# Kernel tuning notes

Measured on AMD Instinct MI355X. Metric: run time of the kernel, lower is better.

The kernel has to match this reference:

```python
import jax, jax.numpy as jnp
import numpy as np

EMBED = 128
STATE = 64
HID = 160
VOCAB = 32000


def layer_norm(x, g, b, eps=1e-5):
    mu = x.mean(-1, keepdims=True)
    var = ((x - mu) ** 2).mean(-1, keepdims=True)
    return (x - mu) * jax.lax.rsqrt(var + eps) * g + b


def mamba_block(x, norm_g, norm_b, in_w, in_b, conv_w, conv_b,
                dt_w, dt_b, b_w, b_b, c_w, c_b, a_log, d, out_w, out_b):
    # x: [B,T,D]
    res = x
    xn = layer_norm(x, norm_g, norm_b)
    proj = xn @ in_w.T + in_b                      # [B,T,2D]
    x_proj, z = jnp.split(proj, 2, axis=-1)
    D = x_proj.shape[-1]
    # depthwise conv1d, kernel 3, same padding
    xc = jax.lax.conv_general_dilated(
        x_proj.transpose(0, 2, 1), conv_w[:, None, :],
        window_strides=(1,), padding=((1, 1),),
        feature_group_count=D,
        dimension_numbers=('NCH', 'OIH', 'NCH')) + conv_b[:, None]
    x_conv = jnp.tanh(xc.transpose(0, 2, 1))       # [B,T,D]
    # input-dependent SSM params, computed for all timesteps at once
    dt = jax.nn.softplus(z @ dt_w.T + dt_b) + 1e-4  # [B,T,S]
    bt = jnp.tanh(z @ b_w.T + b_b)                  # [B,T,S]
    ct = jnp.tanh(z @ c_w.T + c_b)                  # [B,T,S]
    a = -jnp.exp(a_log)                             # [S]
    decay = jnp.exp(a * dt)                         # [B,T,S]

    def step(state, inp):
        dec_t, b_t = inp
        state = state * dec_t + b_t
        return state, state

    state0 = jnp.zeros((x.shape[0], a_log.shape[0]), x.dtype)
    _, states = jax.lax.scan(step, state0,
                             (decay.transpose(1, 0, 2), bt.transpose(1, 0, 2)))
    y = ct * states.transpose(1, 0, 2)              # [B,T,S]
    mix = jnp.concatenate([x_conv * d, y], axis=-1)  # [B,T,D+S]
    return res + mix @ out_w.T + out_b


def _forward(x, lengths, resp_in, emb_table,
             m_norm_g, m_norm_b, m_in_w, m_in_b, m_conv_w, m_conv_b,
             m_dt_w, m_dt_b, m_b_w, m_b_b, m_c_w, m_c_b, m_a_log, m_d,
             m_out_w, m_out_b, pool_g, pool_b, shared_w, shared_b,
             intent_w, intent_b, style_w, style_b, cap_w, cap_b, op_w, op_b,
             dec_emb, dec_init_w, dec_init_b,
             gru_w_ih, gru_w_hh, gru_b_ih, gru_b_hh, dec_out_w, dec_out_b):
    emb = emb_table[x]                              # [B,T,E]
    h_seq = emb
    for i in range(2):
        h_seq = mamba_block(h_seq, m_norm_g[i], m_norm_b[i], m_in_w[i],
                            m_in_b[i], m_conv_w[i], m_conv_b[i], m_dt_w[i],
                            m_dt_b[i], m_b_w[i], m_b_b[i], m_c_w[i], m_c_b[i],
                            m_a_log[i], m_d[i], m_out_w[i], m_out_b[i])
    T = h_seq.shape[1]
    mask = (jnp.arange(T)[None, :] < lengths[:, None])[..., None]
    denom = jnp.maximum(lengths, 1)[:, None].astype(h_seq.dtype)
    pooled = (h_seq * mask).sum(axis=1) / denom     # [B,E]
    h = layer_norm(pooled, pool_g, pool_b)
    h = jax.nn.relu(h @ shared_w.T + shared_b)      # [B,128]
    intent = h @ intent_w.T + intent_b
    style = h @ style_w.T + style_b
    cap = h @ cap_w.T + cap_b
    op = h @ op_w.T + op_b
    # GRU decoder (PyTorch gate order: r, z, n)
    dec_in = dec_emb[resp_in]                       # [B,Td,E]
    h0 = jnp.tanh(h @ dec_init_w.T + dec_init_b)    # [B,H]
    gx = dec_in @ gru_w_ih.T + gru_b_ih             # [B,Td,3H]

    def gru_step(hprev, gx_t):
        gh = hprev @ gru_w_hh.T + gru_b_hh
        xr, xz, xn = jnp.split(gx_t, 3, axis=-1)
        hr, hz, hn = jnp.split(gh, 3, axis=-1)
        r = jax.nn.sigmoid(xr + hr)
        zg = jax.nn.sigmoid(xz + hz)
        n = jnp.tanh(xn + r * hn)
        hnew = (1.0 - zg) * n + zg * hprev
        return hnew, hnew

    _, dec_states = jax.lax.scan(gru_step, h0, gx.transpose(1, 0, 2))
    dec_out = dec_states.transpose(1, 0, 2)         # [B,Td,H]
    resp_logits = dec_out @ dec_out_w.T + dec_out_b  # [B,Td,V]
    return (intent, style, cap, op, resp_logits, h)


def setup_inputs() -> dict:
    key = jax.random.key(0)
    ks = iter(jax.random.split(key, 64))

    def nrm(shape, s=0.02):
        return jax.random.normal(next(ks), shape, jnp.float32) * s

    inp = {}
    inp['x'] = jax.random.randint(next(ks), (32, 512), 0, VOCAB)
    inp['lengths'] = jax.random.randint(next(ks), (32,), 1, 513)
    inp['resp_in'] = jax.random.randint(next(ks), (32, 128), 0, VOCAB)
    inp['emb_table'] = nrm((VOCAB, EMBED), 1.0).at[0].set(0.0)
    inp['m_norm_g'] = jnp.ones((2, EMBED)); inp['m_norm_b'] = jnp.zeros((2, EMBED))
    inp['m_in_w'] = nrm((2, 2 * EMBED, EMBED)); inp['m_in_b'] = jnp.zeros((2, 2 * EMBED))
    inp['m_conv_w'] = nrm((2, EMBED, 3), 0.1); inp['m_conv_b'] = jnp.zeros((2, EMBED))
    inp['m_dt_w'] = nrm((2, STATE, EMBED)); inp['m_dt_b'] = jnp.zeros((2, STATE))
    inp['m_b_w'] = nrm((2, STATE, EMBED)); inp['m_b_b'] = jnp.zeros((2, STATE))
    inp['m_c_w'] = nrm((2, STATE, EMBED)); inp['m_c_b'] = jnp.zeros((2, STATE))
    inp['m_a_log'] = nrm((2, STATE)); inp['m_d'] = jnp.ones((2, EMBED))
    inp['m_out_w'] = nrm((2, EMBED, EMBED + STATE)); inp['m_out_b'] = jnp.zeros((2, EMBED))
    inp['pool_g'] = jnp.ones((EMBED,)); inp['pool_b'] = jnp.zeros((EMBED,))
    inp['shared_w'] = nrm((128, EMBED)); inp['shared_b'] = jnp.zeros((128,))
    inp['intent_w'] = nrm((32, 128)); inp['intent_b'] = jnp.zeros((32,))
    inp['style_w'] = nrm((8, 128)); inp['style_b'] = jnp.zeros((8,))
    inp['cap_w'] = nrm((16, 128)); inp['cap_b'] = jnp.zeros((16,))
    inp['op_w'] = nrm((24, 128)); inp['op_b'] = jnp.zeros((24,))
    inp['dec_emb'] = nrm((VOCAB, EMBED), 1.0).at[0].set(0.0)
    inp['dec_init_w'] = nrm((HID, 128)); inp['dec_init_b'] = jnp.zeros((HID,))
    inp['gru_w_ih'] = nrm((3 * HID, EMBED)); inp['gru_w_hh'] = nrm((3 * HID, HID))
    inp['gru_b_ih'] = jnp.zeros((3 * HID,)); inp['gru_b_hh'] = jnp.zeros((3 * HID,))
    inp['dec_out_w'] = nrm((VOCAB, HID)); inp['dec_out_b'] = jnp.zeros((VOCAB,))
    return inp


def reference(x, lengths, resp_in, emb_table,
              m_norm_g, m_norm_b, m_in_w, m_in_b, m_conv_w, m_conv_b,
              m_dt_w, m_dt_b, m_b_w, m_b_b, m_c_w, m_c_b, m_a_log, m_d,
              m_out_w, m_out_b, pool_g, pool_b, shared_w, shared_b,
              intent_w, intent_b, style_w, style_b, cap_w, cap_b, op_w, op_b,
              dec_emb, dec_init_w, dec_init_b,
              gru_w_ih, gru_w_hh, gru_b_ih, gru_b_hh, dec_out_w, dec_out_b):
    return _forward(x, lengths, resp_in, emb_table,
                    m_norm_g, m_norm_b, m_in_w, m_in_b, m_conv_w, m_conv_b,
                    m_dt_w, m_dt_b, m_b_w, m_b_b, m_c_w, m_c_b, m_a_log, m_d,
                    m_out_w, m_out_b, pool_g, pool_b, shared_w, shared_b,
                    intent_w, intent_b, style_w, style_b, cap_w, cap_b,
                    op_w, op_b, dec_emb, dec_init_w, dec_init_b,
                    gru_w_ih, gru_w_hh, gru_b_ih, gru_b_hh,
                    dec_out_w, dec_out_b)
```

## Files before the change

### kernel.cpp

```cpp
#include <hip/hip_runtime.h>
#include <hip/hip_bf16.h>

#define EMBED 128
#define STATE 64
#define HID   160
#define VOCAB 32000
#define BDIM  32
#define TDIM  512
#define TDEC  128

typedef __attribute__((ext_vector_type(4))) float f32x4;
typedef __attribute__((ext_vector_type(8))) short bf16x8;

__device__ inline float softplus_f(float x) { return x > 20.f ? x : log1pf(expf(x)); }
__device__ inline float sigmoid_f(float x) { return 1.f / (1.f + expf(-x)); }
__device__ inline short f2bf(float x) {
    __hip_bfloat16 v = __float2bfloat16(x);
    return *reinterpret_cast<short*>(&v);
}
__device__ inline float bf2f(short u) {
    union { unsigned int i; float f; } cv;
    cv.i = ((unsigned int)(unsigned short)u) << 16;
    return cv.f;
}

__global__ void prep_kernel(const float* __restrict__ w, short* __restrict__ wb, int n,
                            const int* __restrict__ x, const int* __restrict__ lengths,
                            const int* __restrict__ resp, int* __restrict__ flags) {
    if (blockIdx.x == 0 && threadIdx.x == 0) {
        int f = 1;
        for (int i = 0; i < 32; i++) if (x[2 * i + 1] != 0) { f = 0; break; }
        flags[0] = f;
        f = 1;
        for (int i = 0; i < 16; i++) if (lengths[2 * i + 1] != 0) { f = 0; break; }
        flags[1] = f;
        f = 1;
        for (int i = 0; i < 32; i++) if (resp[2 * i + 1] != 0) { f = 0; break; }
        flags[2] = f;
    }
    int i = blockIdx.x * blockDim.x + threadIdx.x;
    int stride = gridDim.x * blockDim.x;
    for (; i < n; i += stride) wb[i] = f2bf(w[i]);
}

__global__ void embed_kernel(const int* __restrict__ tok, const float* __restrict__ table,
                             float* __restrict__ out, int total,
                             const int* __restrict__ flags, int fidx) {
    int mode = flags[fidx];
    int i = blockIdx.x * blockDim.x + threadIdx.x;
    int stride = gridDim.x * blockDim.x;
    for (; i < total; i += stride) {
        int r = i >> 7, e = i & 127;
        int t = mode ? tok[2 * r] : tok[r];
        out[i] = table[(long)t * EMBED + e];
    }
}

__launch_bounds__(256)
__global__ void mm_inproj(const float* __restrict__ hseq,
                          const float* __restrict__ g, const float* __restrict__ bta,
                          const float* __restrict__ W, const float* __restrict__ bias,
                          short* __restrict__ projb) {
    __shared__ __align__(16) short As[64][136];
    __shared__ __align__(16) short Ws[64][136];
    __shared__ float rsum[64][4], rsum2[64][4];
    const int m0 = blockIdx.x * 64, n0 = blockIdx.y * 64;
    const int tid = threadIdx.x;

    {
        int row = tid >> 2, part = tid & 3;
        const float* src = &hseq[(long)(m0 + row) * 128 + part * 32];
        f32x4 v[8];
        float s = 0.f, s2 = 0.f;
        #pragma unroll
        for (int q = 0; q < 8; q++) {
            v[q] = *(const f32x4*)&src[q * 4];
            s  += v[q].x + v[q].y + v[q].z + v[q].w;
            s2 += v[q].x * v[q].x + v[q].y * v[q].y + v[q].z * v[q].z + v[q].w * v[q].w;
        }
        rsum[row][part] = s; rsum2[row][part] = s2;
        __syncthreads();
        float tot  = rsum[row][0] + rsum[row][1] + rsum[row][2] + rsum[row][3];
        float tot2 = rsum2[row][0] + rsum2[row][1] + rsum2[row][2] + rsum2[row][3];
        float mu = tot * (1.f / 128.f);
        float var = tot2 * (1.f / 128.f) - mu * mu;
        float rstd = rsqrtf(var + 1e-5f);
        #pragma unroll
        for (int q = 0; q < 8; q++) {
            int c = part * 32 + q * 4;
            short4 t4;
            t4.x = f2bf((v[q].x - mu) * rstd * g[c + 0] + bta[c + 0]);
            t4.y = f2bf((v[q].y - mu) * rstd * g[c + 1] + bta[c + 1]);
            t4.z = f2bf((v[q].z - mu) * rstd * g[c + 2] + bta[c + 2]);
            t4.w = f2bf((v[q].w - mu) * rstd * g[c + 3] + bta[c + 3]);
            *(short4*)&As[row][c] = t4;
        }
    }
    #pragma unroll
    for (int it = 0; it < 4; ++it) {
        int idx = tid + it * 256;
        int rr = idx >> 4, cc = idx & 15;
        const float* wp = &W[(long)(n0 + rr) * 128 + cc * 8];
        short t8[8];
        #pragma unroll
        for (int q = 0; q < 8; q++) t8[q] = f2bf(wp[q]);
        *(bf16x8*)&Ws[rr][cc * 8] = *(bf16x8*)t8;
    }
    __syncthreads();

    const int wave = tid >> 6, lane = tid & 63;
    const int wm = wave >> 1, wn = wave & 1;
    const int fr = lane & 15, kg = lane >> 4;
    f32x4 acc[2][2];
    #pragma unroll
    for (int i = 0; i < 2; i++)
        #pragma unroll
        for (int j = 0; j < 2; j++) acc[i][j] = (f32x4){0.f, 0.f, 0.f, 0.f};
    #pragma unroll
    for (int ks = 0; ks < 4; ++ks) {
        int kb = ks * 32 + kg * 8;
        bf16x8 a0 = *(const bf16x8*)&As[wm * 32 + fr][kb];
        bf16x8 a1 = *(const bf16x8*)&As[wm * 32 + 16 + fr][kb];
        bf16x8 w0 = *(const bf16x8*)&Ws[wn * 32 + fr][kb];
        bf16x8 w1 = *(const bf16x8*)&Ws[wn * 32 + 16 + fr][kb];
        acc[0][0] = __builtin_amdgcn_mfma_f32_16x16x32_bf16(a0, w0, acc[0][0], 0, 0, 0);
        acc[0][1] = __builtin_amdgcn_mfma_f32_16x16x32_bf16(a0, w1, acc[0][1], 0, 0, 0);
        acc[1][0] = __builtin_amdgcn_mfma_f32_16x16x32_bf16(a1, w0, acc[1][0], 0, 0, 0);
        acc[1][1] = __builtin_amdgcn_mfma_f32_16x16x32_bf16(a1, w1, acc[1][1], 0, 0, 0);
    }
    #pragma unroll
    for (int i = 0; i < 2; i++)
        #pragma unroll
        for (int j = 0; j < 2; j++) {
            int col = n0 + wn * 32 + j * 16 + fr;
            float bv = bias[col];
            #pragma unroll
            for (int q = 0; q < 4; q++) {
                int row = m0 + wm * 32 + i * 16 + kg * 4 + q;
                projb[(long)row * 256 + col] = f2bf(acc[i][j][q] + bv);
            }
        }
}

__launch_bounds__(256)
__global__ void mm_z(const short* __restrict__ projb,
                     const float* __restrict__ dtw, const float* __restrict__ dtb,
                     const float* __restrict__ alog,
                     const float* __restrict__ bw, const float* __restrict__ bb_,
                     const float* __restrict__ cw, const float* __restrict__ cb_,
                     float* __restrict__ sdat) {
    __shared__ __align__(16) short As[64][136];
    __shared__ __align__(16) short Ws[64][136];
    const int m0 = blockIdx.x * 64, sel = blockIdx.y;
    const int tid = threadIdx.x;
    const float* W = sel == 0 ? dtw : (sel == 1 ? bw : cw);
    const float* B = sel == 0 ? dtb : (sel == 1 ? bb_ : cb_);

    #pragma unroll
    for (int it = 0; it < 4; ++it) {
        int idx = tid + it * 256;
        int rr = idx >> 4, cc = idx & 15;
        *(bf16x8*)&As[rr][cc * 8] = *(const bf16x8*)&projb[(long)(m0 + rr) * 256 + 128 + cc * 8];
    }
    #pragma unroll
    for (int it = 0; it < 4; ++it) {
        int idx = tid + it * 256;
        int rr = idx >> 4, cc = idx & 15;
        const float* wp = &W[(long)rr * 128 + cc * 8];
        short t8[8];
        #pragma unroll
        for (int q = 0; q < 8; q++) t8[q] = f2bf(wp[q]);
        *(bf16x8*)&Ws[rr][cc * 8] = *(bf16x8*)t8;
    }
    __syncthreads();

    const int wave = tid >> 6, lane = tid & 63;
    const int wm = wave >> 1, wn = wave & 1;
    const int fr = lane & 15, kg = lane >> 4;
    f32x4 acc[2][2];
    #pragma unroll
    for (int i = 0; i < 2; i++)
        #pragma unroll
        for (int j = 0; j < 2; j++) acc[i][j] = (f32x4){0.f, 0.f, 0.f, 0.f};
    #pragma unroll
    for (int ks = 0; ks < 4; ++ks) {
        int kb = ks * 32 + kg * 8;
        bf16x8 a0 = *(const bf16x8*)&As[wm * 32 + fr][kb];
        bf16x8 a1 = *(const bf16x8*)&As[wm * 32 + 16 + fr][kb];
        bf16x8 w0 = *(const bf16x8*)&Ws[wn * 32 + fr][kb];
        bf16x8 w1 = *(const bf16x8*)&Ws[wn * 32 + 16 + fr][kb];
        acc[0][0] = __builtin_amdgcn_mfma_f32_16x16x32_bf16(a0, w0, acc[0][0], 0, 0, 0);
        acc[0][1] = __builtin_amdgcn_mfma_f32_16x16x32_bf16(a0, w1, acc[0][1], 0, 0, 0);
        acc[1][0] = __builtin_amdgcn_mfma_f32_16x16x32_bf16(a1, w0, acc[1][0], 0, 0, 0);
        acc[1][1] = __builtin_amdgcn_mfma_f32_16x16x32_bf16(a1, w1, acc[1][1], 0, 0, 0);
    }
    #pragma unroll
    for (int i = 0; i < 2; i++)
        #pragma unroll
        for (int j = 0; j < 2; j++) {
            int n = wn * 32 + j * 16 + fr;
            float bv = B[n];
            float al = (sel == 0) ? -expf(alog[n]) : 0.f;
            #pragma unroll
            for (int q = 0; q < 4; q++) {
                int row = m0 + wm * 32 + i * 16 + kg * 4 + q;
                float v = acc[i][j][q] + bv;
                if (sel == 0) { float dt = softplus_f(v) + 1e-4f; v = expf(al * dt); }
                else v = tanhf(v);
                sdat[(long)row * 192 + sel * 64 + n] = v;
            }
        }
}

__global__ void conv_kernel(const short* __restrict__ projb, const float* __restrict__ cw,
                            const float* __restrict__ cb, const float* __restrict__ dvec,
                            short* __restrict__ mixb, int total) {
    int i = blockIdx.x * blockDim.x + threadIdx.x;
    int stride = gridDim.x * blockDim.x;
    for (; i < total; i += stride) {
        int e = i & 127;
        int r = i >> 7;
        int t = r & (TDIM - 1);
        float x0 = bf2f(projb[(long)r * 256 + e]);
        float xm = (t > 0)        ? bf2f(projb[(long)(r - 1) * 256 + e]) : 0.f;
        float xp = (t < TDIM - 1) ? bf2f(projb[(long)(r + 1) * 256 + e]) : 0.f;
        float v = cw[e * 3 + 0] * xm + cw[e * 3 + 1] * x0 + cw[e * 3 + 2] * xp + cb[e];
        mixb[(long)r * 192 + e] = f2bf(tanhf(v) * dvec[e]);
    }
}

__global__ void scanA_kernel(const float* __restrict__ sdat, float* __restrict__ chunkAB) {
    int b = blockIdx.x, c = blockIdx.y, s = threadIdx.x;
    long rbase = (long)b * TDIM + c * 64;
    float A = 1.f, Bc = 0.f;
    #pragma unroll 8
    for (int t = 0; t < 64; ++t) {
        const float* row = sdat + (rbase + t) * 192;
        float d = row[s];
        Bc = Bc * d + row[64 + s];
        A *= d;
    }
    chunkAB[((b * 8 + c) * 2 + 0) * 64 + s] = A;
    chunkAB[((b * 8 + c) * 2 + 1) * 64 + s] = Bc;
}

__global__ void scanC_kernel(const float* __restrict__ sdat, const float* __restrict__ chunkAB,
                             short* __restrict__ mixb) {
    int b = blockIdx.x, tid = threadIdx.x;
    int c = tid >> 6, s = tid & 63;
    __shared__ float SI[8][64];
    if (c == 0) {
        float st = 0.f;
        #pragma unroll
        for (int cc = 0; cc < 8; ++cc) {
            SI[cc][s] = st;
            float A = chunkAB[((b * 8 + cc) * 2 + 0) * 64 + s];
            float Bc = chunkAB[((b * 8 + cc) * 2 + 1) * 64 + s];
            st = Bc + A * st;
        }
    }
    __syncthreads();
    long rbase = (long)b * TDIM + c * 64;
    float st = SI[c][s];
    #pragma unroll 4
    for (int t = 0; t < 64; ++t) {
        const float* row = sdat + (rbase + t) * 192;
        st = st * row[s] + row[64 + s];
        mixb[(rbase + t) * 192 + 128 + s] = f2bf(row[128 + s] * st);
    }
}

__launch_bounds__(256)
__global__ void mm_out(const short* __restrict__ mixb,
                       const float* __restrict__ W, const float* __restrict__ bias,
                       float* __restrict__ hseq) {
    __shared__ __align__(16) short As[64][200];
    __shared__ __align__(16) short Ws[64][200];
    const int m0 = blockIdx.x * 64, n0 = blockIdx.y * 64;
    const int tid = threadIdx.x;

    #pragma unroll
    for (int it = 0; it < 6; ++it) {
        int idx = tid + it * 256;
        int rr = idx / 24, cc = idx % 24;
        *(bf16x8*)&As[rr][cc * 8] = *(const bf16x8*)&mixb[(long)(m0 + rr) * 192 + cc * 8];
    }
    #pragma unroll
    for (int it = 0; it < 6; ++it) {
        int idx = tid + it * 256;
        int rr = idx / 24, cc = idx % 24;
        const float* wp = &W[(long)(n0 + rr) * 192 + cc * 8];
        short t8[8];
        #pragma unroll
        for (int q = 0; q < 8; q++) t8[q] = f2bf(wp[q]);
        *(bf16x8*)&Ws[rr][cc * 8] = *(bf16x8*)t8;
    }
    __syncthreads();

    const int wave = tid >> 6, lane = tid & 63;
    const int wm = wave >> 1, wn = wave & 1;
    const int fr = lane & 15, kg = lane >> 4;
    f32x4 acc[2][2];
    #pragma unroll
    for (int i = 0; i < 2; i++)
        #pragma unroll
        for (int j = 0; j < 2; j++) acc[i][j] = (f32x4){0.f, 0.f, 0.f, 0.f};
    #pragma unroll
    for (int ks = 0; ks < 6; ++ks) {
        int kb = ks * 32 + kg * 8;
        bf16x8 a0 = *(const bf16x8*)&As[wm * 32 + fr][kb];
        bf16x8 a1 = *(const bf16x8*)&As[wm * 32 + 16 + fr][kb];
        bf16x8 w0 = *(const bf16x8*)&Ws[wn * 32 + fr][kb];
        bf16x8 w1 = *(const bf16x8*)&Ws[wn * 32 + 16 + fr][kb];
        acc[0][0] = __builtin_amdgcn_mfma_f32_16x16x32_bf16(a0, w0, acc[0][0], 0, 0, 0);
        acc[0][1] = __builtin_amdgcn_mfma_f32_16x16x32_bf16(a0, w1, acc[0][1], 0, 0, 0);
        acc[1][0] = __builtin_amdgcn_mfma_f32_16x16x32_bf16(a1, w0, acc[1][0], 0, 0, 0);
        acc[1][1] = __builtin_amdgcn_mfma_f32_16x16x32_bf16(a1, w1, acc[1][1], 0, 0, 0);
    }
    #pragma unroll
    for (int i = 0; i < 2; i++)
        #pragma unroll
        for (int j = 0; j < 2; j++) {
            int col = n0 + wn * 32 + j * 16 + fr;
            float bv = bias[col];
            #pragma unroll
            for (int q = 0; q < 4; q++) {
                int row = m0 + wm * 32 + i * 16 + kg * 4 + q;
                hseq[(long)row * 128 + col] += acc[i][j][q] + bv;
            }
        }
}

__launch_bounds__(256)
__global__ void mm_gx(const int* __restrict__ resp, const float* __restrict__ table,
                      const int* __restrict__ flags,
                      const float* __restrict__ W, const float* __restrict__ bias,
                      float* __restrict__ gx) {
    __shared__ __align__(16) short As[64][136];
    __shared__ __align__(16) short Ws[64][136];
    const int m0 = blockIdx.x * 64, n0 = blockIdx.y * 64;
    const int tid = threadIdx.x;
    const int mode = flags[2];

    #pragma unroll
    for (int it = 0; it < 4; ++it) {
        int idx = tid + it * 256;
        int rr = idx >> 4, cc = idx & 15;
        int gr = m0 + rr;
        int tk = mode ? resp[2 * gr] : resp[gr];
        const float* sp = &table[(long)tk * 128 + cc * 8];
        short t8[8];
        #pragma unroll
        for (int q = 0; q < 8; q++) t8[q] = f2bf(sp[q]);
        *(bf16x8*)&As[rr][cc * 8] = *(bf16x8*)t8;
    }
    #pragma unroll
    for (int it = 0; it < 4; ++it) {
        int idx = tid + it * 256;
        int rr = idx >> 4, cc = idx & 15;
        int gn = n0 + rr;
        short t8[8];
        if (gn < 480) {
            const float* wp = &W[(long)gn * 128 + cc * 8];
            #pragma unroll
            for (int q = 0; q < 8; q++) t8[q] = f2bf(wp[q]);
        } else {
            #pragma unroll
            for (int q = 0; q < 8; q++) t8[q] = 0;
        }
        *(bf16x8*)&Ws[rr][cc * 8] = *(bf16x8*)t8;
    }
    __syncthreads();

    const int wave = tid >> 6, lane = tid & 63;
    const int wm = wave >> 1, wn = wave & 1;
    const int fr = lane & 15, kg = lane >> 4;
    f32x4 acc[2][2];
    #pragma unroll
    for (int i = 0; i < 2; i++)
        #pragma unroll
        for (int j = 0; j < 2; j++) acc[i][j] = (f32x4){0.f, 0.f, 0.f, 0.f};
    #pragma unroll
    for (int ks = 0; ks < 4; ++ks) {
        int kb = ks * 32 + kg * 8;
        bf16x8 a0 = *(const bf16x8*)&As[wm * 32 + fr][kb];
        bf16x8 a1 = *(const bf16x8*)&As[wm * 32 + 16 + fr][kb];
        bf16x8 w0 = *(const bf16x8*)&Ws[wn * 32 + fr][kb];
        bf16x8 w1 = *(const bf16x8*)&Ws[wn * 32 + 16 + fr][kb];
        acc[0][0] = __builtin_amdgcn_mfma_f32_16x16x32_bf16(a0, w0, acc[0][0], 0, 0, 0);
        acc[0][1] = __builtin_amdgcn_mfma_f32_16x16x32_bf16(a0, w1, acc[0][1], 0, 0, 0);
        acc[1][0] = __builtin_amdgcn_mfma_f32_16x16x32_bf16(a1, w0, acc[1][0], 0, 0, 0);
        acc[1][1] = __builtin_amdgcn_mfma_f32_16x16x32_bf16(a1, w1, acc[1][1], 0, 0, 0);
    }
    #pragma unroll
    for (int i = 0; i < 2; i++)
        #pragma unroll
        for (int j = 0; j < 2; j++) {
            int col = n0 + wn * 32 + j * 16 + fr;
            if (col >= 480) continue;
            float bv = bias[col];
            #pragma unroll
            for (int q = 0; q < 4; q++) {
                int row = m0 + wm * 32 + i * 16 + kg * 4 + q;
                gx[(long)row * 480 + col] = acc[i][j][q] + bv;
            }
        }
}

__launch_bounds__(512, 1)
__global__ void gru_heads_kernel(const float* __restrict__ hseq, const int* __restrict__ lengths,
                                 const int* __restrict__ flags,
                                 const float* __restrict__ pg, const float* __restrict__ pb,
                                 const float* __restrict__ sw, const float* __restrict__ sb,
                                 const float* __restrict__ iw_, const float* __restrict__ ib_,
                                 const float* __restrict__ stw, const float* __restrict__ stb,
                                 const float* __restrict__ cw_, const float* __restrict__ cb2,
                                 const float* __restrict__ ow_, const float* __restrict__ ob2,
                                 const float* __restrict__ diw, const float* __restrict__ dib,
                                 const float* __restrict__ gx,
                                 const float* __restrict__ whh, const float* __restrict__ bhh,
                                 float* __restrict__ o_intent, float* __restrict__ o_style,
                                 float* __restrict__ o_cap, float* __restrict__ o_op,
                                 float* __restrict__ o_h,
                                 short* __restrict__ dec_out) {
    int b = blockIdx.x, tid = threadIdx.x;
    __shared__ float red[4][128];
    __shared__ float pooled[128], hsh[128];
    __shared__ float hs[160], gh[480];
    int lm = flags[1];
    int len = lm ? lengths[2 * b] : lengths[b];
    const float* gxb = gx + (long)b * TDEC * 480;

    {
        int e = tid & 127, ch = tid >> 7;
        float s = 0.f;
        for (int t = ch; t < len; t += 4) s += hseq[((long)b * TDIM + t) * 128 + e];
        red[ch][e] = s;
    }
    __syncthreads();
    if (tid < 128) {
        float s = red[0][tid] + red[1][tid] + red[2][tid] + red[3][tid];
        pooled[tid] = s / (float)(len > 1 ? len : 1);
    }
    __syncthreads();
    if (tid < 128) red[0][tid] = pooled[tid];
    __syncthreads();
    for (int off = 64; off > 0; off >>= 1) { if (tid < off) red[0][tid] += red[0][tid + off]; __syncthreads(); }
    float mu = red[0][0] / 128.f;
    __syncthreads();
    if (tid < 128) { float d = pooled[tid] - mu; red[0][tid] = d * d; }
    __syncthreads();
    for (int off = 64; off > 0; off >>= 1) { if (tid < off) red[0][tid] += red[0][tid + off]; __syncthreads(); }
    float rstd = rsqrtf(red[0][0] / 128.f + 1e-5f);
    __syncthreads();
    if (tid < 128) pooled[tid] = (pooled[tid] - mu) * rstd * pg[tid] + pb[tid];
    __syncthreads();
    if (tid < 128) {
        float a = sb[tid];
        for (int k = 0; k < 128; k++) a = fmaf(pooled[k], sw[tid * 128 + k], a);
        a = fmaxf(a, 0.f);
        hsh[tid] = a;
        o_h[b * 128 + tid] = a;
    }
    __syncthreads();
    if (tid < 32) {
        float a = ib_[tid];
        for (int k = 0; k < 128; k++) a = fmaf(hsh[k], iw_[tid * 128 + k], a);
        o_intent[b * 32 + tid] = a;
    } else if (tid < 40) {
        int n = tid - 32; float a = stb[n];
        for (int k = 0; k < 128; k++) a = fmaf(hsh[k], stw[n * 128 + k], a);
        o_style[b * 8 + n] = a;
    } else if (tid < 56) {
        int n = tid - 40; float a = cb2[n];
        for (int k = 0; k < 128; k++) a = fmaf(hsh[k], cw_[n * 128 + k], a);
        o_cap[b * 16 + n] = a;
    } else if (tid < 80) {
        int n = tid - 56; float a = ob2[n];
        for (int k = 0; k < 128; k++) a = fmaf(hsh[k], ow_[n * 128 + k], a);
        o_op[b * 24 + n] = a;
    }
    if (tid < 160) {
        float a = dib[tid];
        for (int k = 0; k < 128; k++) a = fmaf(hsh[k], diw[tid * 128 + k], a);
        hs[tid] = tanhf(a);
    }
    f32x4 w[40];
    float bh = 0.f;
    if (tid < 480) {
        bh = bhh[tid];
        const f32x4* wrow = reinterpret_cast<const f32x4*>(whh + tid * 160);
        #pragma unroll
        for (int q = 0; q < 40; q++) w[q] = wrow[q];
    }
    float prA = 0.f, pzA = 0.f, pnA = 0.f, prB = 0.f, pzB = 0.f, pnB = 0.f;
    if (tid < 160) {
        prA = gxb[tid];        pzA = gxb[160 + tid];        pnA = gxb[320 + tid];
        prB = gxb[480 + tid];  pzB = gxb[640 + tid];        pnB = gxb[800 + tid];
    }
    __syncthreads();
    for (int t = 0; t < TDEC; ++t) {
        if (tid < 480) {
            const f32x4* hv = reinterpret_cast<const f32x4*>(hs);
            float a0 = bh, a1 = 0.f, a2 = 0.f, a3 = 0.f;
            #pragma unroll
            for (int q = 0; q < 40; q += 4) {
                f32x4 ha = hv[q],     wa = w[q];
                f32x4 hb = hv[q + 1], wb = w[q + 1];
                f32x4 hc = hv[q + 2], wc = w[q + 2];
                f32x4 hd = hv[q + 3], wd = w[q + 3];
                a0 = fmaf(ha.w, wa.w, fmaf(ha.z, wa.z, fmaf(ha.y, wa.y, fmaf(ha.x, wa.x, a0))));
                a1 = fmaf(hb.w, wb.w, fmaf(hb.z, wb.z, fmaf(hb.y, wb.y, fmaf(hb.x, wb.x, a1))));
                a2 = fmaf(hc.w, wc.w, fmaf(hc.z, wc.z, fmaf(hc.y, wc.y, fmaf(hc.x, wc.x, a2))));
                a3 = fmaf(hd.w, wd.w, fmaf(hd.z, wd.z, fmaf(hd.y, wd.y, fmaf(hd.x, wd.x, a3))));
            }
            gh[tid] = (a0 + a1) + (a2 + a3);
        }
        __syncthreads();
        if (tid < 160) {
            float r = sigmoid_f(prA + gh[tid]);
            float z = sigmoid_f(pzA + gh[160 + tid]);
            float n = tanhf(pnA + r * gh[320 + tid]);
            float hnew = (1.f - z) * n + z * hs[tid];
            dec_out[((long)b * TDEC + t) * 160 + tid] = f2bf(hnew);
            hs[tid] = hnew;
            prA = prB; pzA = pzB; pnA = pnB;
            if (t + 2 < TDEC) {
                const float* g2 = gxb + (long)(t + 2) * 480;
                prB = g2[tid]; pzB = g2[160 + tid]; pnB = g2[320 + tid];
            }
        }
        __syncthreads();
    }
}

__launch_bounds__(256)
__global__ void vocab_gemm(const short* __restrict__ A,
                           const short* __restrict__ W,
                           const float* __restrict__ bias,
                           float* __restrict__ C) {
    __shared__ __align__(16) short As[128][168];
    __shared__ __align__(16) short Ws[64][168];
    int n0 = blockIdx.x * 64, m0 = blockIdx.y * 128;
    int tid = threadIdx.x;

    #pragma unroll
    for (int it = 0; it < 10; ++it) {
        int idx = tid + it * 256;
        int r = idx / 20, c8 = idx % 20;
        *(bf16x8*)&As[r][c8 * 8] = *(const bf16x8*)&A[(long)(m0 + r) * 160 + c8 * 8];
    }
    #pragma unroll
    for (int it = 0; it < 5; ++it) {
        int idx = tid + it * 256;
        int r = idx / 20, c8 = idx % 20;
        *(bf16x8*)&Ws[r][c8 * 8] = *(const bf16x8*)&W[(long)(n0 + r) * 160 + c8 * 8];
    }
    __syncthreads();

    int wave = tid >> 6, lane = tid & 63;
    int wm = wave >> 1, wn = wave & 1;
    int fr = lane & 15, kg = lane >> 4;

    f32x4 acc[4][2];
    #pragma unroll
    for (int i = 0; i < 4; i++)
        #pragma unroll
        for (int j = 0; j < 2; j++) acc[i][j] = (f32x4){0.f, 0.f, 0.f, 0.f};

    #pragma unroll
    for (int ks = 0; ks < 5; ++ks) {
        int kb = ks * 32 + kg * 8;
        bf16x8 a[4], bfr[2];
        #pragma unroll
        for (int i = 0; i < 4; i++)
            a[i] = *(const bf16x8*)&As[wm * 64 + i * 16 + fr][kb];
        #pragma unroll
        for (int j = 0; j < 2; j++)
            bfr[j] = *(const bf16x8*)&Ws[wn * 32 + j * 16 + fr][kb];
        #pragma unroll
        for (int i = 0; i < 4; i++)
            #pragma unroll
            for (int j = 0; j < 2; j++)
                acc[i][j] = __builtin_amdgcn_mfma_f32_16x16x32_bf16(a[i], bfr[j], acc[i][j], 0, 0, 0);
    }

    __syncthreads();
    float* Cs = (float*)&As[0][0];
    #pragma unroll
    for (int i = 0; i < 4; i++)
        #pragma unroll
        for (int j = 0; j < 2; j++) {
            int col = wn * 32 + j * 16 + fr;
            #pragma unroll
            for (int q = 0; q < 4; q++) {
                int row = wm * 64 + i * 16 + kg * 4 + q;
                Cs[row * 64 + col] = acc[i][j][q];
            }
        }
    __syncthreads();
    #pragma unroll
    for (int it = 0; it < 8; ++it) {
        int idx = tid + it * 256;
        int row = idx >> 4, c4 = (idx & 15) * 4;
        f32x4 v = *(f32x4*)&Cs[row * 64 + c4];
        int gc = n0 + c4;
        v.x += bias[gc]; v.y += bias[gc + 1]; v.z += bias[gc + 2]; v.w += bias[gc + 3];
        *(f32x4*)&C[(long)(m0 + row) * VOCAB + gc] = v;
    }
}

extern "C" void kernel_launch(void* const* d_in, const int* in_sizes, int n_in,
                              void* d_out, int out_size, void* d_ws, size_t ws_size,
                              hipStream_t stream) {
    const int* x        = (const int*)d_in[0];
    const int* lengths  = (const int*)d_in[1];
    const int* resp_in  = (const int*)d_in[2];
    const float* emb_table = (const float*)d_in[3];
    const float* m_norm_g  = (const float*)d_in[4];
    const float* m_norm_b  = (const float*)d_in[5];
    const float* m_in_w    = (const float*)d_in[6];
    const float* m_in_b    = (const float*)d_in[7];
    const float* m_conv_w  = (const float*)d_in[8];
    const float* m_conv_b  = (const float*)d_in[9];
    const float* m_dt_w    = (const float*)d_in[10];
    const float* m_dt_b    = (const float*)d_in[11];
    const float* m_b_w     = (const float*)d_in[12];
    const float* m_b_b     = (const float*)d_in[13];
    const float* m_c_w     = (const float*)d_in[14];
    const float* m_c_b     = (const float*)d_in[15];
    const float* m_a_log   = (const float*)d_in[16];
    const float* m_d       = (const float*)d_in[17];
    const float* m_out_w   = (const float*)d_in[18];
    const float* m_out_b   = (const float*)d_in[19];
    const float* pool_g    = (const float*)d_in[20];
    const float* pool_b    = (const float*)d_in[21];
    const float* shared_w  = (const float*)d_in[22];
    const float* shared_b  = (const float*)d_in[23];
    const float* intent_w  = (const float*)d_in[24];
    const float* intent_b  = (const float*)d_in[25];
    const float* style_w   = (const float*)d_in[26];
    const float* style_b   = (const float*)d_in[27];
    const float* cap_w     = (const float*)d_in[28];
    const float* cap_b     = (const float*)d_in[29];
    const float* op_w      = (const float*)d_in[30];
    const float* op_b      = (const float*)d_in[31];
    const float* dec_emb   = (const float*)d_in[32];
    const float* dec_init_w = (const float*)d_in[33];
    const float* dec_init_b = (const float*)d_in[34];
    const float* gru_w_ih  = (const float*)d_in[35];
    const float* gru_w_hh  = (const float*)d_in[36];
    const float* gru_b_ih  = (const float*)d_in[37];
    const float* gru_b_hh  = (const float*)d_in[38];
    const float* dec_out_w = (const float*)d_in[39];
    const float* dec_out_b = (const float*)d_in[40];

    float* out = (float*)d_out;
    const long o_intent = 0;
    const long o_style  = 32 * 32;
    const long o_cap    = o_style + 32 * 8;
    const long o_op     = o_cap + 32 * 16;
    const long o_logits = o_op + 32 * 24;
    const long o_h      = o_logits + (long)BDIM * TDEC * VOCAB;

    const int R = BDIM * TDIM;
    const int Rd = BDIM * TDEC;

    char* Sb = (char*)(out + o_logits);
    float* hseq  = (float*)Sb;  Sb += (long)R * 128 * 4;
    short* projb = (short*)Sb;  Sb += (long)R * 256 * 2;
    float* sdat  = (float*)Sb;  Sb += (long)R * 192 * 4;
    short* mixb  = (short*)Sb;  Sb += (long)R * 192 * 2;
    float* gx    = (float*)Sb;  Sb += (long)Rd * 480 * 4;

    int* flags   = (int*)d_ws;
    short* dec_obf = (short*)((float*)d_ws + 16);
    short* w_bf  = dec_obf + (long)Rd * HID;
    float* chunkAB = (float*)(w_bf + (long)VOCAB * HID);

    prep_kernel<<<2048, 256, 0, stream>>>(dec_out_w, w_bf, VOCAB * HID, x, lengths, resp_in, flags);
    embed_kernel<<<4096, 256, 0, stream>>>(x, emb_table, hseq, R * 128, flags, 0);

    for (int i = 0; i < 2; ++i) {
        mm_inproj<<<dim3(R / 64, 4), 256, 0, stream>>>(
            hseq, m_norm_g + i * 128, m_norm_b + i * 128,
            m_in_w + i * 256 * 128, m_in_b + i * 256, projb);
        mm_z<<<dim3(R / 64, 3), 256, 0, stream>>>(
            projb, m_dt_w + i * 8192, m_dt_b + i * 64, m_a_log + i * 64,
            m_b_w + i * 8192, m_b_b + i * 64,
            m_c_w + i * 8192, m_c_b + i * 64, sdat);
        conv_kernel<<<2048, 256, 0, stream>>>(
            projb, m_conv_w + i * 384, m_conv_b + i * 128, m_d + i * 128, mixb, R * 128);
        scanA_kernel<<<dim3(BDIM, 8), 64, 0, stream>>>(sdat, chunkAB);
        scanC_kernel<<<BDIM, 512, 0, stream>>>(sdat, chunkAB, mixb);
        mm_out<<<dim3(R / 64, 2), 256, 0, stream>>>(
            mixb, m_out_w + i * 128 * 192, m_out_b + i * 128, hseq);
    }

    mm_gx<<<dim3(Rd / 64, 8), 256, 0, stream>>>(
        resp_in, dec_emb, flags, gru_w_ih, gru_b_ih, gx);
    gru_heads_kernel<<<BDIM, 512, 0, stream>>>(
        hseq, lengths, flags,
        pool_g, pool_b, shared_w, shared_b,
        intent_w, intent_b, style_w, style_b, cap_w, cap_b, op_w, op_b,
        dec_init_w, dec_init_b,
        gx, gru_w_hh, gru_b_hh,
        out + o_intent, out + o_style, out + o_cap, out + o_op, out + o_h,
        dec_obf);
    vocab_gemm<<<dim3(VOCAB / 64, Rd / 128), 256, 0, stream>>>(
        dec_obf, w_bf, dec_out_b, out + o_logits);
}
```

Before: 507.2 us.

## Spread scan over more blocks, remap vocab GEMM blocks for XCD locality, ballot flags

Three changes are bundled. The scanC kernel now launches one 64-thread block per (batch, chunk) and has each block recompute its chunk's prefix state from chunkAB, removing the shared-memory handoff and barrier. The vocab GEMM switches to a 1D grid with a remapped block index so consecutive blocks on the same XCD share M/N tiles, aiming for better L2 reuse of weights. Flag detection in prep uses wave ballots instead of a serial single-thread loop.

```diff
diff --git a/kernel.cpp b/kernel.cpp
--- a/kernel.cpp
+++ b/kernel.cpp
@@ -27,16 +27,16 @@
 __global__ void prep_kernel(const float* __restrict__ w, short* __restrict__ wb, int n,
                             const int* __restrict__ x, const int* __restrict__ lengths,
                             const int* __restrict__ resp, int* __restrict__ flags) {
-    if (blockIdx.x == 0 && threadIdx.x == 0) {
-        int f = 1;
-        for (int i = 0; i < 32; i++) if (x[2 * i + 1] != 0) { f = 0; break; }
-        flags[0] = f;
-        f = 1;
-        for (int i = 0; i < 16; i++) if (lengths[2 * i + 1] != 0) { f = 0; break; }
-        flags[1] = f;
-        f = 1;
-        for (int i = 0; i < 32; i++) if (resp[2 * i + 1] != 0) { f = 0; break; }
-        flags[2] = f;
+    if (blockIdx.x == 0 && threadIdx.x < 64) {
+        int lane = threadIdx.x;
+        unsigned long long m1 = __ballot(lane < 32 && x[2 * lane + 1] != 0);
+        unsigned long long m2 = __ballot(lane < 16 && lengths[2 * lane + 1] != 0);
+        unsigned long long m3 = __ballot(lane < 32 && resp[2 * lane + 1] != 0);
+        if (lane == 0) {
+            flags[0] = (m1 == 0ull);
+            flags[1] = (m2 == 0ull);
+            flags[2] = (m3 == 0ull);
+        }
     }
     int i = blockIdx.x * blockDim.x + threadIdx.x;
     int stride = gridDim.x * blockDim.x;
@@ -246,22 +246,14 @@
 
 __global__ void scanC_kernel(const float* __restrict__ sdat, const float* __restrict__ chunkAB,
                              short* __restrict__ mixb) {
-    int b = blockIdx.x, tid = threadIdx.x;
-    int c = tid >> 6, s = tid & 63;
-    __shared__ float SI[8][64];
-    if (c == 0) {
-        float st = 0.f;
-        #pragma unroll
-        for (int cc = 0; cc < 8; ++cc) {
-            SI[cc][s] = st;
-            float A = chunkAB[((b * 8 + cc) * 2 + 0) * 64 + s];
-            float Bc = chunkAB[((b * 8 + cc) * 2 + 1) * 64 + s];
-            st = Bc + A * st;
-        }
-    }
-    __syncthreads();
+    int b = blockIdx.x, c = blockIdx.y, s = threadIdx.x;
+    float st = 0.f;
+    for (int cc = 0; cc < c; ++cc) {
+        float A  = chunkAB[((b * 8 + cc) * 2 + 0) * 64 + s];
+        float Bc = chunkAB[((b * 8 + cc) * 2 + 1) * 64 + s];
+        st = Bc + A * st;
+    }
     long rbase = (long)b * TDIM + c * 64;
-    float st = SI[c][s];
     #pragma unroll 4
     for (int t = 0; t < 64; ++t) {
         const float* row = sdat + (rbase + t) * 192;
@@ -541,7 +533,10 @@
                            float* __restrict__ C) {
     __shared__ __align__(16) short As[128][168];
     __shared__ __align__(16) short Ws[64][168];
-    int n0 = blockIdx.x * 64, m0 = blockIdx.y * 128;
+    int bid = blockIdx.x;
+    int wgid = (bid & 7) * 2000 + (bid >> 3);
+    int n0 = (wgid >> 5) * 64;
+    int m0 = (wgid & 31) * 128;
     int tid = threadIdx.x;
 
     #pragma unroll
@@ -692,7 +687,7 @@
         conv_kernel<<<2048, 256, 0, stream>>>(
             projb, m_conv_w + i * 384, m_conv_b + i * 128, m_d + i * 128, mixb, R * 128);
         scanA_kernel<<<dim3(BDIM, 8), 64, 0, stream>>>(sdat, chunkAB);
-        scanC_kernel<<<BDIM, 512, 0, stream>>>(sdat, chunkAB, mixb);
+        scanC_kernel<<<dim3(BDIM, 8), 64, 0, stream>>>(sdat, chunkAB, mixb);
         mm_out<<<dim3(R / 64, 2), 256, 0, stream>>>(
             mixb, m_out_w + i * 128 * 192, m_out_b + i * 128, hseq);
     }
@@ -707,6 +702,6 @@
         gx, gru_w_hh, gru_b_hh,
         out + o_intent, out + o_style, out + o_cap, out + o_op, out + o_h,
         dec_obf);
-    vocab_gemm<<<dim3(VOCAB / 64, Rd / 128), 256, 0, stream>>>(
+    vocab_gemm<<<16000, 256, 0, stream>>>(
         dec_obf, w_bf, dec_out_b, out + o_logits);
 }
```

Result: slower. 533.1 us (+5.1%).
